# Kernel tuning notes

Measured on AMD Instinct MI355X. Metric: run time of the kernel, lower is better.

## Reference

```python
import jax, jax.numpy as jnp
import numpy as np
from jax import lax

NUM_CLASSES = 80
TOPK = 1000
CONF_THRESH = 0.05
NMS_THRESH = 0.6
MAX_COORD = 4096.0  # > any box coordinate; used for class-aware NMS offset trick
N_ANCHORS = 262144


def setup_inputs() -> dict:
    key = jax.random.key(0)
    k1, k2, k3 = jax.random.split(key, 3)
    # classification logits; shift down so sigmoid scores are mostly below conf_thresh
    cls_pred = jax.random.normal(k1, (1, N_ANCHORS, NUM_CLASSES), jnp.float32) * 2.0 - 2.0
    # valid xyxy boxes in absolute pixel coords (image ~1024)
    xy = jax.random.uniform(k2, (1, N_ANCHORS, 2), jnp.float32) * 1000.0
    wh = jax.random.uniform(k3, (1, N_ANCHORS, 2), jnp.float32) * 200.0 + 4.0
    box_pred = jnp.concatenate([xy, xy + wh], axis=-1)
    return {"cls_pred": cls_pred, "box_pred": box_pred, "img_h": 1024, "img_w": 1024}


def _pairwise_iou(b):
    # b: [K, 4] xyxy -> [K, K] IoU
    x1, y1, x2, y2 = b[:, 0], b[:, 1], b[:, 2], b[:, 3]
    area = (x2 - x1) * (y2 - y1)
    ix1 = jnp.maximum(x1[:, None], x1[None, :])
    iy1 = jnp.maximum(y1[:, None], y1[None, :])
    ix2 = jnp.minimum(x2[:, None], x2[None, :])
    iy2 = jnp.minimum(y2[:, None], y2[None, :])
    inter = jnp.clip(ix2 - ix1, 0.0) * jnp.clip(iy2 - iy1, 0.0)
    return inter / (area[:, None] + area[None, :] - inter + 1e-9)


def reference(cls_pred, box_pred, img_h, img_w):
    cls_p = cls_pred[0]          # [N, C]
    box_p = box_pred[0]          # [N, 4]
    # sigmoid + flatten + descending sort + slice(topk)  ==  top_k on flat scores
    scores_all = jax.nn.sigmoid(cls_p).reshape(-1)            # [N*C]
    top_scores, top_idxs = lax.top_k(scores_all, TOPK)        # sorted descending
    valid = top_scores > CONF_THRESH                          # keep mask (fixed size)
    labels = top_idxs % NUM_CLASSES
    anchor_idxs = top_idxs // NUM_CLASSES
    boxes = box_p[anchor_idxs]                                # [K, 4]

    # class-aware (per-class) greedy NMS via coordinate offset trick
    offset = labels.astype(boxes.dtype)[:, None] * MAX_COORD
    iou = _pairwise_iou(boxes + offset)                       # [K, K]
    idx = jnp.arange(TOPK)

    def body(i, keep):
        sup = keep[i] & (iou[i] > NMS_THRESH) & (idx > i)
        return keep & ~sup

    keep = lax.fori_loop(0, TOPK, body, valid)

    # normalize boxes to [0, 1] by image size and clip (as inference_single_image)
    scale = jnp.array([img_w, img_h, img_w, img_h], dtype=boxes.dtype)
    boxes_norm = jnp.clip(boxes / scale, 0.0, 1.0)

    scores_out = jnp.where(keep, top_scores, 0.0)
    return boxes_norm, scores_out, labels, keep
```

## Files before the change

### kernel.cpp

```cpp
#include <hip/hip_runtime.h>
#include <stdint.h>

#define NUM_CLASSES 80u
#define TOPK 1000
#define CONF_T 0.05f
#define NMS_T 0.6f
#define MAX_COORD 4096.0f
#define TARGET 1152u
#define CAP 49152u
#define SRVCAP 2048u
#define STATIC_F 4.0f
#define STATIC_KEY 0xC0800000u
#define NBINS 4096
#define BINSH 13
#define LCAP 512u
#define PBLK 1024u

typedef unsigned long long ull;
typedef ull ull2 __attribute__((ext_vector_type(2)));

__device__ __forceinline__ uint32_t fkey(float x) {
  uint32_t k = __float_as_uint(x);
  return (k & 0x80000000u) ? ~k : (k | 0x80000000u);
}

__device__ __forceinline__ uint32_t suffix_scan_256(uint32_t v, uint32_t* part,
                                                    int t) {
  int lane = t & 63, wid = t >> 6;
#pragma unroll
  for (int off = 1; off < 64; off <<= 1) {
    uint32_t x = __shfl_down(v, off);
    if (lane + off < 64) v += x;
  }
  if (lane == 0) part[wid] = v;
  __syncthreads();
  if (wid == 0 && lane < 4) {
    uint32_t pv = part[lane];
#pragma unroll
    for (int off = 1; off < 4; off <<= 1) {
      uint32_t x = __shfl_down(pv, off);
      if (lane + off < 4) pv += x;
    }
    part[lane] = pv;
  }
  __syncthreads();
  uint32_t after = (wid < 3) ? part[wid + 1] : 0u;
  return v + after;
}

template <int NBINSX>
__device__ __forceinline__ void pick_bin(const uint32_t* hl, uint32_t target,
                                         int t, uint32_t* part, uint32_t* binS,
                                         uint32_t* AS, uint32_t* cntS) {
  const int CH = NBINSX / 256;
  uint32_t s = 0;
#pragma unroll
  for (int j = 0; j < CH; ++j) s += hl[t * CH + j];
  uint32_t incl = suffix_scan_256(s, part, t);
  uint32_t after = incl - s;
  if (incl >= target && after < target) {
    uint32_t cum = after;
    for (int j = CH - 1; j >= 0; --j) {
      uint32_t h = hl[t * CH + j];
      if (cum + h >= target) { *binS = (uint32_t)(t * CH + j); *AS = cum; *cntS = h; break; }
      cum += h;
    }
  }
}

__global__ void __launch_bounds__(256) kz(uint32_t* hist, uint32_t* sel,
                                          float* out, float* topScore) {
  int g = blockIdx.x * 256 + threadIdx.x;
  hist[g] = 0u;
  if (g < 16) sel[g] = 0u;
  for (int i = g; i < 4000; i += 4096) out[i] = 0.0f;
  if (g < 1000) { out[5000 + g] = 0.0f; topScore[g] = 0.0f; }
}

__global__ void __launch_bounds__(256) kA(const float4* __restrict__ cls, int n4,
                                          uint32_t* __restrict__ sel,
                                          uint32_t* __restrict__ hist,
                                          uint32_t* __restrict__ candKey,
                                          uint32_t* __restrict__ candIdx) {
  __shared__ uint32_t lk[LCAP];
  __shared__ uint32_t li[LCAP];
  __shared__ uint32_t lcnt, gbase;
  if (threadIdx.x == 0) lcnt = 0u;
  __syncthreads();
  int stride = gridDim.x * blockDim.x;
  for (int i = blockIdx.x * blockDim.x + threadIdx.x; i < n4; i += stride) {
    float4 v = cls[i];
    float f4[4] = {v.x, v.y, v.z, v.w};
#pragma unroll
    for (int c = 0; c < 4; ++c) {
      if (f4[c] >= STATIC_F) {
        uint32_t k = fkey(f4[c]);
        uint32_t b = (k - STATIC_KEY) >> BINSH; if (b > NBINS - 1u) b = NBINS - 1u;
        atomicAdd(&hist[b], 1u);
        uint32_t p = atomicAdd(&lcnt, 1u);
        if (p < LCAP) { lk[p] = k; li[p] = (uint32_t)i * 4u + c; }
        else {
          uint32_t gp = atomicAdd(&sel[2], 1u);
          if (gp < CAP) { candKey[gp] = k; candIdx[gp] = (uint32_t)i * 4u + c; }
        }
      }
    }
  }
  __syncthreads();
  uint32_t c = lcnt; if (c > LCAP) c = LCAP;
  if (threadIdx.x == 0 && c) gbase = atomicAdd(&sel[2], c);
  __syncthreads();
  for (uint32_t i = threadIdx.x; i < c; i += 256u) {
    uint32_t gp = gbase + i;
    if (gp < CAP) { candKey[gp] = lk[i]; candIdx[gp] = li[i]; }
  }
}

__global__ void __launch_bounds__(256) kSel(
    const float4* __restrict__ cls4, int n4,
    uint32_t* __restrict__ sel, const uint32_t* __restrict__ hist,
    const uint32_t* __restrict__ candKey, const uint32_t* __restrict__ candIdx,
    ull* __restrict__ srv) {
  __shared__ uint32_t hl[NBINS];
  __shared__ uint32_t part[16];
  __shared__ uint32_t sk_[PBLK];
  __shared__ uint32_t si_[PBLK];
  __shared__ uint32_t lcnt, gbase, binS, AS, cntS;
  int t = threadIdx.x;
  uint32_t n = sel[2];
  bool fb = (n < TARGET) || (n > CAP);

  if (!fb) {
    for (int i = t; i < NBINS; i += 256) hl[i] = hist[i];
    if (t == 0) { lcnt = 0u; binS = 0u; AS = 0u; cntS = 0u; }
    __syncthreads();
    pick_bin<NBINS>(hl, TARGET, t, part, &binS, &AS, &cntS);
    __syncthreads();
    uint32_t T;
    if (AS + cntS > SRVCAP)
      T = STATIC_KEY + ((binS + 1u) << BINSH);
    else
      T = STATIC_KEY + (binS << BINSH);
    uint32_t stride = gridDim.x * blockDim.x;
    for (uint32_t i = blockIdx.x * 256u + (uint32_t)t; i < n; i += stride) {
      uint32_t k = candKey[i];
      if (k >= T) {
        uint32_t p = atomicAdd(&lcnt, 1u);
        if (p < PBLK) { sk_[p] = k; si_[p] = candIdx[i]; }
      }
    }
    __syncthreads();
    uint32_t c = lcnt; if (c > PBLK) c = PBLK;
    if (t == 0 && c) gbase = atomicAdd(&sel[4], c);
    __syncthreads();
    for (uint32_t i = t; i < c; i += 256u) {
      uint32_t k = sk_[i];
      float x = __uint_as_float(k & 0x7fffffffu);
      float p = 1.0f / (1.0f + expf(-x));
      uint32_t pos = gbase + i;
      if (pos < SRVCAP)
        srv[pos] = ((ull)__float_as_uint(p) << 32) | (ull)(uint32_t)(~si_[i]);
    }
  } else {
    if (blockIdx.x != 0) return;
    for (int i = t; i < NBINS; i += 256) hl[i] = 0u;
    if (t == 0) { binS = 0u; AS = 0u; cntS = 0u; }
    __syncthreads();
    for (int i = t; i < n4; i += 256) {
      float4 v = cls4[i];
      atomicAdd(&hl[fkey(v.x) >> 20], 1u);
      atomicAdd(&hl[fkey(v.y) >> 20], 1u);
      atomicAdd(&hl[fkey(v.z) >> 20], 1u);
      atomicAdd(&hl[fkey(v.w) >> 20], 1u);
    }
    __syncthreads();
    pick_bin<NBINS>(hl, TARGET, t, part, &binS, &AS, &cntS);
    __syncthreads();
    uint32_t b20 = binS, A = AS;
    for (int i = t; i < 1024; i += 256) hl[i] = 0u;
    if (t == 0) { binS = 0u; }
    __syncthreads();
    for (int i = t; i < n4; i += 256) {
      float4 v = cls4[i];
      uint32_t k4[4] = {fkey(v.x), fkey(v.y), fkey(v.z), fkey(v.w)};
#pragma unroll
      for (int c2 = 0; c2 < 4; ++c2)
        if ((k4[c2] >> 20) == b20) atomicAdd(&hl[(k4[c2] >> 10) & 1023u], 1u);
    }
    __syncthreads();
    uint32_t rem = TARGET - A;
    pick_bin<1024>(hl, rem, t, part, &binS, &AS, &cntS);
    __syncthreads();
    uint32_t T = (b20 << 20) | (binS << 10);
    for (int i = t; i < n4; i += 256) {
      float4 v = cls4[i];
      uint32_t k4[4] = {fkey(v.x), fkey(v.y), fkey(v.z), fkey(v.w)};
#pragma unroll
      for (int c2 = 0; c2 < 4; ++c2) {
        uint32_t k = k4[c2];
        if (k >= T) {
          uint32_t pos = atomicAdd(&sel[4], 1u);
          if (pos < SRVCAP) {
            float x = (k & 0x80000000u) ? __uint_as_float(k & 0x7fffffffu)
                                        : __uint_as_float(~k);
            float p = 1.0f / (1.0f + expf(-x));
            uint32_t idx = (uint32_t)i * 4u + c2;
            srv[pos] = ((ull)__float_as_uint(p) << 32) | (ull)(uint32_t)(~idx);
          }
        }
      }
    }
  }
}

__global__ void __launch_bounds__(64) kF2(
    const float* __restrict__ box, const int* __restrict__ ph,
    const int* __restrict__ pw, const uint32_t* __restrict__ sel,
    const ull* __restrict__ srv, float* __restrict__ out,
    float* __restrict__ topScore, float* __restrict__ obox) {
  __shared__ __align__(16) ull sk[SRVCAP];
  int t = threadIdx.x;
  uint32_t scount = sel[4]; if (scount > SRVCAP) scount = SRVCAP;
  uint32_t pad = (scount + 1u) & ~1u;
  for (uint32_t i = t; i < pad; i += 64u) sk[i] = (i < scount) ? srv[i] : 0ull;
  __syncthreads();
  uint32_t i = blockIdx.x * 64u + (uint32_t)t;
  if (i >= scount) return;
  ull my = sk[i];
  uint32_t rank = 0;
#pragma unroll 4
  for (uint32_t j = 0; j < pad; j += 2u) {
    ull2 v = *reinterpret_cast<const ull2*>(&sk[j]);
    rank += (v.x > my) + (v.y > my);
  }
  if (rank >= TOPK) return;
  uint32_t idx = ~(uint32_t)my;
  float p = __uint_as_float((uint32_t)(my >> 32));
  uint32_t label = idx % NUM_CLASSES;
  uint32_t anchor = idx / NUM_CLASSES;
  float W = (float)pw[0], H = (float)ph[0];
  float b0 = box[anchor * 4u + 0u], b1 = box[anchor * 4u + 1u];
  float b2 = box[anchor * 4u + 2u], b3 = box[anchor * 4u + 3u];
  out[rank * 4 + 0] = fminf(fmaxf(b0 / W, 0.0f), 1.0f);
  out[rank * 4 + 1] = fminf(fmaxf(b1 / H, 0.0f), 1.0f);
  out[rank * 4 + 2] = fminf(fmaxf(b2 / W, 0.0f), 1.0f);
  out[rank * 4 + 3] = fminf(fmaxf(b3 / H, 0.0f), 1.0f);
  out[5000 + rank] = (float)label;
  topScore[rank] = p;
  float off = (float)label * MAX_COORD;
  obox[rank * 4 + 0] = b0 + off; obox[rank * 4 + 1] = b1 + off;
  obox[rank * 4 + 2] = b2 + off; obox[rank * 4 + 3] = b3 + off;
}

__global__ void kG(const float* __restrict__ obox, ull* __restrict__ masks) {
  int i = blockIdx.x;
  float x1i = obox[i * 4 + 0], y1i = obox[i * 4 + 1];
  float x2i = obox[i * 4 + 2], y2i = obox[i * 4 + 3];
  float ai = (x2i - x1i) * (y2i - y1i);
  for (int base = 0; base < 1024; base += 256) {
    int jj = base + (int)threadIdx.x;
    bool bit = false;
    if (jj < TOPK && jj > i) {
      float x1j = obox[jj * 4 + 0], y1j = obox[jj * 4 + 1];
      float x2j = obox[jj * 4 + 2], y2j = obox[jj * 4 + 3];
      float aj = (x2j - x1j) * (y2j - y1j);
      float ix1 = fmaxf(x1i, x1j), iy1 = fmaxf(y1i, y1j);
      float ix2 = fminf(x2i, x2j), iy2 = fminf(y2i, y2j);
      float iw = fmaxf(ix2 - ix1, 0.0f), ih = fmaxf(iy2 - iy1, 0.0f);
      float inter = iw * ih;
      float iou = inter / (ai + aj - inter + 1e-9f);
      bit = iou > NMS_T;
    }
    ull m = __ballot(bit);
    if ((threadIdx.x & 63u) == 0u) masks[i * 16 + (jj >> 6)] = m;
  }
}

__global__ void __launch_bounds__(256) kH(const float* __restrict__ topScore,
                                          const ull* __restrict__ masks,
                                          float* __restrict__ out) {
  __shared__ ull lmask[TOPK * 16];
  __shared__ uint32_t nzrow[TOPK];
  __shared__ ull keepsh[16];
  int t = threadIdx.x;
  for (int i = t; i < TOPK; i += 256) nzrow[i] = 0u;
  if (t < 16) keepsh[t] = 0ull;
  __syncthreads();
  for (int i = t; i < TOPK * 16; i += 256) {
    ull m = masks[i];
    lmask[i] = m;
    if (m) atomicOr(&nzrow[i >> 4], 1u);
  }
  for (int base = 0; base < 1024; base += 256) {
    int r = base + t;
    bool v = (r < TOPK) && (topScore[r] > CONF_T);
    ull b = __ballot(v);
    if ((t & 63) == 0) keepsh[(base >> 6) + (t >> 6)] = b;
  }
  __syncthreads();
  if (t < 64) {
    ull kw = (t < 16) ? keepsh[t] : 0ull;
    ull nzw = 0ull;
    if (t < 16) {
      for (int b = 0; b < 64; ++b) {
        int r = t * 64 + b;
        if (r < TOPK && nzrow[r]) nzw |= 1ull << b;
      }
    }
    for (int w = 0; w < 16; ++w) {
      ull cur = __shfl(kw, w) & __shfl(nzw, w);
      while (cur) {
        int b = __ffsll((long long)cur) - 1;
        int i = w * 64 + b;
        if (t < 16) kw &= ~lmask[i * 16 + t];
        ull nk = __shfl(kw, w);
        cur = nk & __shfl(nzw, w);
        cur &= (b == 63) ? 0ull : (~0ull << (b + 1));
      }
    }
    if (t < 16) keepsh[t] = kw;
  }
  __syncthreads();
  for (int r = t; r < TOPK; r += 256) {
    bool k = (keepsh[r >> 6] >> (r & 63)) & 1ull;
    float s = topScore[r];
    out[4000 + r] = k ? s : 0.0f;
    out[6000 + r] = k ? 1.0f : 0.0f;
  }
}

extern "C" void kernel_launch(void* const* d_in, const int* in_sizes, int n_in,
                              void* d_out, int out_size, void* d_ws, size_t ws_size,
                              hipStream_t stream) {
  const float* cls = (const float*)d_in[0];
  const float* box = (const float*)d_in[1];
  const int* ph = (const int*)d_in[2];
  const int* pw = (const int*)d_in[3];
  float* out = (float*)d_out;
  int n = in_sizes[0];

  uint8_t* w = (uint8_t*)d_ws;
  uint32_t* hist    = (uint32_t*)(w);
  uint32_t* sel     = (uint32_t*)(w + 16384);
  uint32_t* candKey = (uint32_t*)(w + 20480);
  uint32_t* candIdx = (uint32_t*)(w + 20480 + (size_t)CAP * 4);
  ull*      srv     = (ull*)     (w + 20480 + (size_t)CAP * 8);
  float*    topScore= (float*)   (w + 20480 + (size_t)CAP * 8 + 16384);
  float*    obox    = (float*)   (w + 20480 + (size_t)CAP * 8 + 16384 + 4096);
  ull*      masks   = (ull*)     (w + 20480 + (size_t)CAP * 8 + 16384 + 4096 + 16384);

  kz  <<<16, 256, 0, stream>>>(hist, sel, out, topScore);
  kA  <<<1024, 256, 0, stream>>>((const float4*)cls, n / 4, sel, hist, candKey, candIdx);
  kSel<<<64, 256, 0, stream>>>((const float4*)cls, n / 4, sel, hist, candKey, candIdx, srv);
  kF2 <<<SRVCAP / 64, 64, 0, stream>>>(box, ph, pw, sel, srv, out, topScore, obox);
  kG  <<<TOPK, 256, 0, stream>>>(obox, masks);
  kH  <<<1, 256, 0, stream>>>(topScore, masks, out);
}
```

Before: 210.2 us.

## Move candidate histogram into kSel shared memory and skip empty NMS mask rows

Removes the global histogram atomics from the streaming kA pass; each kSel block instead rebuilds the histogram from the compacted candidate keys in shared memory. kG now records a per-row bitmask of nonzero mask words so kH loads only nonzero words and no longer needs shared atomics to find active rows. kA grid is doubled and kF2 uses 256-thread blocks. Every kSel block redundantly scans all candidates to build its histogram, which adds work when the candidate count is large.

After: 192.5 us. 8.4% less time.

```diff
diff --git a/kernel.cpp b/kernel.cpp
--- a/kernel.cpp
+++ b/kernel.cpp
@@ -68,10 +68,9 @@
   }
 }
 
-__global__ void __launch_bounds__(256) kz(uint32_t* hist, uint32_t* sel,
-                                          float* out, float* topScore) {
+__global__ void __launch_bounds__(256) kz(uint32_t* sel, float* out,
+                                          float* topScore) {
   int g = blockIdx.x * 256 + threadIdx.x;
-  hist[g] = 0u;
   if (g < 16) sel[g] = 0u;
   for (int i = g; i < 4000; i += 4096) out[i] = 0.0f;
   if (g < 1000) { out[5000 + g] = 0.0f; topScore[g] = 0.0f; }
@@ -79,7 +78,6 @@
 
 __global__ void __launch_bounds__(256) kA(const float4* __restrict__ cls, int n4,
                                           uint32_t* __restrict__ sel,
-                                          uint32_t* __restrict__ hist,
                                           uint32_t* __restrict__ candKey,
                                           uint32_t* __restrict__ candIdx) {
   __shared__ uint32_t lk[LCAP];
@@ -94,14 +92,11 @@
 #pragma unroll
     for (int c = 0; c < 4; ++c) {
       if (f4[c] >= STATIC_F) {
-        uint32_t k = fkey(f4[c]);
-        uint32_t b = (k - STATIC_KEY) >> BINSH; if (b > NBINS - 1u) b = NBINS - 1u;
-        atomicAdd(&hist[b], 1u);
         uint32_t p = atomicAdd(&lcnt, 1u);
-        if (p < LCAP) { lk[p] = k; li[p] = (uint32_t)i * 4u + c; }
+        if (p < LCAP) { lk[p] = fkey(f4[c]); li[p] = (uint32_t)i * 4u + c; }
         else {
           uint32_t gp = atomicAdd(&sel[2], 1u);
-          if (gp < CAP) { candKey[gp] = k; candIdx[gp] = (uint32_t)i * 4u + c; }
+          if (gp < CAP) { candKey[gp] = fkey(f4[c]); candIdx[gp] = (uint32_t)i * 4u + c; }
         }
       }
     }
@@ -118,7 +113,7 @@
 
 __global__ void __launch_bounds__(256) kSel(
     const float4* __restrict__ cls4, int n4,
-    uint32_t* __restrict__ sel, const uint32_t* __restrict__ hist,
+    uint32_t* __restrict__ sel,
     const uint32_t* __restrict__ candKey, const uint32_t* __restrict__ candIdx,
     ull* __restrict__ srv) {
   __shared__ uint32_t hl[NBINS];
@@ -131,8 +126,25 @@
   bool fb = (n < TARGET) || (n > CAP);
 
   if (!fb) {
-    for (int i = t; i < NBINS; i += 256) hl[i] = hist[i];
+    for (int i = t; i < NBINS; i += 256) hl[i] = 0u;
     if (t == 0) { lcnt = 0u; binS = 0u; AS = 0u; cntS = 0u; }
+    __syncthreads();
+    const uint4* ck4 = (const uint4*)candKey;
+    uint32_t n4c = n >> 2;
+    for (uint32_t i = t; i < n4c; i += 256u) {
+      uint4 kv = ck4[i];
+      uint32_t b0 = (kv.x - STATIC_KEY) >> BINSH; if (b0 > NBINS - 1u) b0 = NBINS - 1u;
+      uint32_t b1 = (kv.y - STATIC_KEY) >> BINSH; if (b1 > NBINS - 1u) b1 = NBINS - 1u;
+      uint32_t b2 = (kv.z - STATIC_KEY) >> BINSH; if (b2 > NBINS - 1u) b2 = NBINS - 1u;
+      uint32_t b3 = (kv.w - STATIC_KEY) >> BINSH; if (b3 > NBINS - 1u) b3 = NBINS - 1u;
+      atomicAdd(&hl[b0], 1u); atomicAdd(&hl[b1], 1u);
+      atomicAdd(&hl[b2], 1u); atomicAdd(&hl[b3], 1u);
+    }
+    for (uint32_t i = (n4c << 2) + (uint32_t)t; i < n; i += 256u) {
+      uint32_t b = (candKey[i] - STATIC_KEY) >> BINSH;
+      if (b > NBINS - 1u) b = NBINS - 1u;
+      atomicAdd(&hl[b], 1u);
+    }
     __syncthreads();
     pick_bin<NBINS>(hl, TARGET, t, part, &binS, &AS, &cntS);
     __syncthreads();
@@ -213,7 +225,7 @@
   }
 }
 
-__global__ void __launch_bounds__(64) kF2(
+__global__ void __launch_bounds__(256) kF2(
     const float* __restrict__ box, const int* __restrict__ ph,
     const int* __restrict__ pw, const uint32_t* __restrict__ sel,
     const ull* __restrict__ srv, float* __restrict__ out,
@@ -222,9 +234,9 @@
   int t = threadIdx.x;
   uint32_t scount = sel[4]; if (scount > SRVCAP) scount = SRVCAP;
   uint32_t pad = (scount + 1u) & ~1u;
-  for (uint32_t i = t; i < pad; i += 64u) sk[i] = (i < scount) ? srv[i] : 0ull;
-  __syncthreads();
-  uint32_t i = blockIdx.x * 64u + (uint32_t)t;
+  for (uint32_t i = t; i < pad; i += 256u) sk[i] = (i < scount) ? srv[i] : 0ull;
+  __syncthreads();
+  uint32_t i = blockIdx.x * 256u + (uint32_t)t;
   if (i >= scount) return;
   ull my = sk[i];
   uint32_t rank = 0;
@@ -252,8 +264,12 @@
   obox[rank * 4 + 2] = b2 + off; obox[rank * 4 + 3] = b3 + off;
 }
 
-__global__ void kG(const float* __restrict__ obox, ull* __restrict__ masks) {
+__global__ void kG(const float* __restrict__ obox, ull* __restrict__ masks,
+                   uint32_t* __restrict__ rowsum) {
+  __shared__ uint32_t rsS;
   int i = blockIdx.x;
+  if (threadIdx.x == 0) rsS = 0u;
+  __syncthreads();
   float x1i = obox[i * 4 + 0], y1i = obox[i * 4 + 1];
   float x2i = obox[i * 4 + 2], y2i = obox[i * 4 + 3];
   float ai = (x2i - x1i) * (y2i - y1i);
@@ -272,24 +288,28 @@
       bit = iou > NMS_T;
     }
     ull m = __ballot(bit);
-    if ((threadIdx.x & 63u) == 0u) masks[i * 16 + (jj >> 6)] = m;
-  }
+    if ((threadIdx.x & 63u) == 0u) {
+      masks[i * 16 + (jj >> 6)] = m;
+      if (m) atomicOr(&rsS, 1u << (jj >> 6));
+    }
+  }
+  __syncthreads();
+  if (threadIdx.x == 0) rowsum[i] = rsS;
 }
 
 __global__ void __launch_bounds__(256) kH(const float* __restrict__ topScore,
                                           const ull* __restrict__ masks,
+                                          const uint32_t* __restrict__ rowsum,
                                           float* __restrict__ out) {
   __shared__ ull lmask[TOPK * 16];
-  __shared__ uint32_t nzrow[TOPK];
+  __shared__ uint32_t rsL[TOPK];
   __shared__ ull keepsh[16];
   int t = threadIdx.x;
-  for (int i = t; i < TOPK; i += 256) nzrow[i] = 0u;
+  for (int i = t; i < TOPK; i += 256) rsL[i] = rowsum[i];
   if (t < 16) keepsh[t] = 0ull;
   __syncthreads();
   for (int i = t; i < TOPK * 16; i += 256) {
-    ull m = masks[i];
-    lmask[i] = m;
-    if (m) atomicOr(&nzrow[i >> 4], 1u);
+    lmask[i] = ((rsL[i >> 4] >> (i & 15)) & 1u) ? masks[i] : 0ull;
   }
   for (int base = 0; base < 1024; base += 256) {
     int r = base + t;
@@ -304,7 +324,7 @@
     if (t < 16) {
       for (int b = 0; b < 64; ++b) {
         int r = t * 64 + b;
-        if (r < TOPK && nzrow[r]) nzw |= 1ull << b;
+        if (r < TOPK && rsL[r]) nzw |= 1ull << b;
       }
     }
     for (int w = 0; w < 16; ++w) {
@@ -340,7 +360,6 @@
   int n = in_sizes[0];
 
   uint8_t* w = (uint8_t*)d_ws;
-  uint32_t* hist    = (uint32_t*)(w);
   uint32_t* sel     = (uint32_t*)(w + 16384);
   uint32_t* candKey = (uint32_t*)(w + 20480);
   uint32_t* candIdx = (uint32_t*)(w + 20480 + (size_t)CAP * 4);
@@ -348,11 +367,12 @@
   float*    topScore= (float*)   (w + 20480 + (size_t)CAP * 8 + 16384);
   float*    obox    = (float*)   (w + 20480 + (size_t)CAP * 8 + 16384 + 4096);
   ull*      masks   = (ull*)     (w + 20480 + (size_t)CAP * 8 + 16384 + 4096 + 16384);
-
-  kz  <<<16, 256, 0, stream>>>(hist, sel, out, topScore);
-  kA  <<<1024, 256, 0, stream>>>((const float4*)cls, n / 4, sel, hist, candKey, candIdx);
-  kSel<<<64, 256, 0, stream>>>((const float4*)cls, n / 4, sel, hist, candKey, candIdx, srv);
-  kF2 <<<SRVCAP / 64, 64, 0, stream>>>(box, ph, pw, sel, srv, out, topScore, obox);
-  kG  <<<TOPK, 256, 0, stream>>>(obox, masks);
-  kH  <<<1, 256, 0, stream>>>(topScore, masks, out);
-}
+  uint32_t* rowsum  = (uint32_t*)(w + 20480 + (size_t)CAP * 8 + 16384 + 4096 + 16384 + 131072);
+
+  kz  <<<16, 256, 0, stream>>>(sel, out, topScore);
+  kA  <<<2048, 256, 0, stream>>>((const float4*)cls, n / 4, sel, candKey, candIdx);
+  kSel<<<64, 256, 0, stream>>>((const float4*)cls, n / 4, sel, candKey, candIdx, srv);
+  kF2 <<<SRVCAP / 256, 256, 0, stream>>>(box, ph, pw, sel, srv, out, topScore, obox);
+  kG  <<<TOPK, 256, 0, stream>>>(obox, masks, rowsum);
+  kH  <<<1, 256, 0, stream>>>(topScore, masks, rowsum, out);
+}
```
